# Performance work log

Measured on AMD Instinct MI355X. Metric: run time of the kernel, lower is better.

Reference implementation:

```python
import jax, jax.numpy as jnp
import numpy as np

B, S, DM, H = 8, 512, 1024, 16
D = DM // H            # head_dim = 64
NFEAT = 4              # len(feature_types)
N_DIST = 2 * 512 - 1   # max_utt_num*2-1 = 1023
N_DISC = 16 + 1        # len(DISCOURSE_RELATIONS)+1
N_COOC = 5 + 1


def setup_inputs() -> dict:
    key = jax.random.key(0)
    ks = jax.random.split(key, 24)
    inp = {}
    inp["query"] = jax.random.normal(ks[0], (B, S, DM), jnp.float32)
    inp["key"] = jax.random.normal(ks[1], (B, S, DM), jnp.float32)
    inp["value"] = jax.random.normal(ks[2], (B, S, DM), jnp.float32)
    inp["distance_adj"] = jax.random.randint(ks[3], (B, S, S), 0, N_DIST).astype(jnp.int32)
    inp["speaker_adj"] = jax.random.uniform(ks[4], (B, S, S), jnp.float32)
    inp["discourse_adj"] = jax.random.randint(ks[5], (B, S, S), 0, N_DISC).astype(jnp.int32)
    inp["cooccurrence_adj"] = jax.random.randint(ks[6], (B, S, S), 0, N_COOC).astype(jnp.int32)
    inp["mask"] = jnp.ones((B, 1, 1, S), jnp.int32)
    w = lambda k, shape: jax.random.normal(k, shape, jnp.float32) * 0.02
    inp["Wq"] = w(ks[7], (DM, DM)); inp["bq"] = jnp.zeros((DM,), jnp.float32)
    inp["Wk"] = w(ks[8], (DM, DM)); inp["bk"] = jnp.zeros((DM,), jnp.float32)
    inp["Wv"] = w(ks[9], (DM, DM)); inp["bv"] = jnp.zeros((DM,), jnp.float32)
    inp["Wo"] = w(ks[10], (DM, DM)); inp["bo"] = jnp.zeros((DM,), jnp.float32)
    inp["dist_embed"] = w(ks[11], (N_DIST, 1))
    inp["disc_embed"] = w(ks[12], (N_DISC, 1)).at[0].set(0.0)  # padding_idx=0
    inp["cooc_embed"] = w(ks[13], (N_COOC, 1)).at[0].set(0.0)  # padding_idx=0
    inp["fcw"] = w(ks[14], (H, NFEAT))       # per-head 1x1 conv weights
    inp["fcb"] = jnp.zeros((H,), jnp.float32)
    inp["cw"] = w(ks[15], (2,))              # combine conv weights
    inp["cb"] = jnp.zeros((), jnp.float32)
    return inp


def reference(query, key, value, distance_adj, speaker_adj, discourse_adj,
              cooccurrence_adj, mask, Wq, bq, Wk, bk, Wv, bv, Wo, bo,
              dist_embed, disc_embed, cooc_embed, fcw, fcb, cw, cb):
    scale = jnp.asarray(D ** 0.5, query.dtype)
    # Linear projections, split heads -> [B, H, S, D]
    split = lambda x: x.reshape(B, S, H, D).transpose(0, 2, 1, 3)
    Q = split(query @ Wq.T + bq)
    K = split(key @ Wk.T + bk)
    V = split(value @ Wv.T + bv)
    energy = jnp.einsum('bhqd,bhkd->bhqk', Q, K) / scale  # [B,H,S,S]
    # Adjacency feature maps in feature_types order: distance, speaker, discourse, cooccurrence
    dist = dist_embed[distance_adj, 0]
    disc = disc_embed[discourse_adj, 0] * (discourse_adj != 0)
    cooc = cooc_embed[cooccurrence_adj, 0] * (cooccurrence_adj != 0)
    feature_map = jnp.stack([dist, speaker_adj, disc, cooc], axis=1)  # [B,4,S,S]
    # Per-head 1x1 conv over the 4 feature channels + relu
    feat = jax.nn.relu(jnp.einsum('hc,bcij->bhij', fcw, feature_map)
                       + fcb[None, :, None, None])       # [B,H,S,S]
    # Combine conv (1x1, 2 channels -> 1) + relu
    energy = jax.nn.relu(cw[0] * energy + cw[1] * feat + cb)
    energy = jnp.where(mask == 0, -jnp.inf, energy)
    attention = jax.nn.softmax(energy, axis=-1)           # [B,H,S,S]
    x = jnp.einsum('bhqk,bhkd->bhqd', attention, V)       # dropout p=0 (eval)
    x = x.transpose(0, 2, 1, 3).reshape(B, S, DM)
    x = x @ Wo.T + bo
    return x, attention
```

## Files before the change

kernel.cpp:

```cpp
#include <hip/hip_runtime.h>

using short8 = __attribute__((ext_vector_type(8))) short;
using f32x4  = __attribute__((ext_vector_type(4))) float;
typedef unsigned short u16x4 __attribute__((ext_vector_type(4)));

__device__ __forceinline__ unsigned short f2bf(float x) {
    union { float f; unsigned u; } v; v.f = x;
    unsigned u = v.u;
    unsigned r = (u + 0x7fffu + ((u >> 16) & 1u)) >> 16;
    return (unsigned short)r;
}
__device__ __forceinline__ float bf2f(unsigned short h) {
    union { unsigned u; float f; } v; v.u = ((unsigned)h) << 16;
    return v.f;
}

__device__ __forceinline__ void async16(const void* g, void* l) {
    __builtin_amdgcn_global_load_lds(
        (const __attribute__((address_space(1))) void*)g,
        (__attribute__((address_space(3))) void*)l, 16, 0, 0);
}

__global__ __launch_bounds__(256) void cvt_qkv(
    const float* __restrict__ q, const float* __restrict__ k, const float* __restrict__ v,
    unsigned short* __restrict__ dst)
{
    int z = blockIdx.z;
    const float* src = (z == 0) ? q : ((z == 1) ? k : v);
    unsigned short* o = dst + (size_t)z * 4194304;
    size_t i = ((size_t)blockIdx.x * 256 + threadIdx.x) * 8;
    float4 a = *(const float4*)(src + i);
    float4 b = *(const float4*)(src + i + 4);
    ushort4 lo, hi;
    lo.x = f2bf(a.x); lo.y = f2bf(a.y); lo.z = f2bf(a.z); lo.w = f2bf(a.w);
    hi.x = f2bf(b.x); hi.y = f2bf(b.y); hi.z = f2bf(b.z); hi.w = f2bf(b.w);
    *(ushort4*)(o + i) = lo;
    *(ushort4*)(o + i + 4) = hi;
}

__global__ __launch_bounds__(256) void cvt_w(
    const float* __restrict__ wq, const float* __restrict__ wk,
    const float* __restrict__ wv, const float* __restrict__ wo,
    unsigned short* __restrict__ dst)
{
    int z = blockIdx.z;
    const float* src = (z == 0) ? wq : ((z == 1) ? wk : ((z == 2) ? wv : wo));
    unsigned short* o = dst + (size_t)z * 1048576;
    size_t i = ((size_t)blockIdx.x * 256 + threadIdx.x) * 8;
    float4 a = *(const float4*)(src + i);
    float4 b = *(const float4*)(src + i + 4);
    ushort4 lo, hi;
    lo.x = f2bf(a.x); lo.y = f2bf(a.y); lo.z = f2bf(a.z); lo.w = f2bf(a.w);
    hi.x = f2bf(b.x); hi.y = f2bf(b.y); hi.z = f2bf(b.z); hi.w = f2bf(b.w);
    *(ushort4*)(o + i) = lo;
    *(ushort4*)(o + i + 4) = hi;
}

__global__ __launch_bounds__(256) void feat_kernel(
    const int* __restrict__ dist_adj, const float* __restrict__ spk,
    const int* __restrict__ disc_adj, const int* __restrict__ cooc_adj,
    const float* __restrict__ dist_emb, const float* __restrict__ disc_emb,
    const float* __restrict__ cooc_emb, const float* __restrict__ fcw,
    const float* __restrict__ fcb, const float* __restrict__ cw,
    unsigned short* __restrict__ G)
{
    __shared__ float s_dist[1023];
    __shared__ float s_disc[17];
    __shared__ float s_cooc[6];
    __shared__ float s_fcw[64];
    __shared__ float s_fcb[16];
    int tid = threadIdx.x;
    for (int i = tid; i < 1023; i += 256) s_dist[i] = dist_emb[i];
    if (tid < 17) s_disc[tid] = disc_emb[tid];
    if (tid < 6)  s_cooc[tid] = cooc_emb[tid];
    if (tid < 64) s_fcw[tid]  = fcw[tid];
    if (tid < 16) s_fcb[tid]  = fcb[tid];
    __syncthreads();
    float cw1 = cw[1];

    int bx = blockIdx.x;
    int k  = (bx & 1) * 256 + tid;
    int qq = (bx >> 1) & 127;
    int b  = bx >> 8;

    size_t abase = ((size_t)b * 512 + qq * 4) * 512 + k;
    float f0[4], f1[4], f2[4], f3[4];
#pragma unroll
    for (int r = 0; r < 4; ++r) {
        size_t a = abase + (size_t)r * 512;
        int dd = dist_adj[a];
        f1[r]  = spk[a];
        int dc = disc_adj[a];
        int cc = cooc_adj[a];
        f0[r] = s_dist[dd];
        f2[r] = dc ? s_disc[dc] : 0.f;
        f3[r] = cc ? s_cooc[cc] : 0.f;
    }

    size_t gq = ((size_t)b * 16 * 128 + qq) * 512 + k;
#pragma unroll
    for (int h = 0; h < 16; ++h) {
        float w0 = s_fcw[h*4+0], w1 = s_fcw[h*4+1], w2 = s_fcw[h*4+2], w3 = s_fcw[h*4+3];
        float bb = s_fcb[h];
        ushort4 o;
        o.x = f2bf(fmaxf(w0*f0[0] + w1*f1[0] + w2*f2[0] + w3*f3[0] + bb, 0.f) * cw1);
        o.y = f2bf(fmaxf(w0*f0[1] + w1*f1[1] + w2*f2[1] + w3*f3[1] + bb, 0.f) * cw1);
        o.z = f2bf(fmaxf(w0*f0[2] + w1*f1[2] + w2*f2[2] + w3*f3[2] + bb, 0.f) * cw1);
        o.w = f2bf(fmaxf(w0*f0[3] + w1*f1[3] + w2*f2[3] + w3*f3[3] + bb, 0.f) * cw1);
        *(ushort4*)(G + (gq + (size_t)h * 65536) * 4) = o;
    }
}

template<int OMODE>
__device__ __forceinline__ void gemm_bf16_body(
    const unsigned short* __restrict__ A, const unsigned short* __restrict__ W,
    const float* __restrict__ bias, void* __restrict__ outp, int m0, int n0)
{
    __shared__ __align__(16) unsigned short As[128 * 32];
    __shared__ __align__(16) unsigned short Bs[128 * 32];
    int tid = threadIdx.x;
    int lane = tid & 63, wid = tid >> 6;
    int wx = wid & 1, wy = wid >> 1;
    int lanelo = lane & 15, hi8 = (lane >> 4) * 8;
    int rowc = lane >> 2;
    int colc = (lane & 3) * 8;

    f32x4 acc[4][4];
#pragma unroll
    for (int i = 0; i < 4; ++i)
#pragma unroll
        for (int j = 0; j < 4; ++j) {
            acc[i][j][0] = 0.f; acc[i][j][1] = 0.f; acc[i][j][2] = 0.f; acc[i][j][3] = 0.f;
        }

    for (int kk = 0; kk < 32; ++kk) {
        int k0 = kk * 32;
        __syncthreads();
#pragma unroll
        for (int p = 0; p < 2; ++p) {
            int c = 2 * wid + p;
            int row = c * 16 + rowc;
            async16(A + (size_t)(m0 + row) * 1024 + k0 + colc, As + c * 512);
        }
#pragma unroll
        for (int p = 0; p < 2; ++p) {
            int c = 2 * wid + p;
            int row = c * 16 + rowc;
            async16(W + (size_t)(n0 + row) * 1024 + k0 + colc, Bs + c * 512);
        }
        __syncthreads();

        short8 af[4], bfr[4];
#pragma unroll
        for (int i = 0; i < 4; ++i)
            af[i] = *(const short8*)(As + (wy*64 + i*16 + lanelo) * 32 + hi8);
#pragma unroll
        for (int j = 0; j < 4; ++j)
            bfr[j] = *(const short8*)(Bs + (wx*64 + j*16 + lanelo) * 32 + hi8);
#pragma unroll
        for (int i = 0; i < 4; ++i)
#pragma unroll
            for (int j = 0; j < 4; ++j)
                acc[i][j] = __builtin_amdgcn_mfma_f32_16x16x32_bf16(af[i], bfr[j], acc[i][j], 0, 0, 0);
    }

    float bia[4];
#pragma unroll
    for (int j = 0; j < 4; ++j) bia[j] = bias[n0 + wx*64 + j*16 + lanelo];
#pragma unroll
    for (int i = 0; i < 4; ++i) {
        int mbase = m0 + wy*64 + i*16 + (lane >> 4) * 4;
#pragma unroll
        for (int j = 0; j < 4; ++j) {
            int n = n0 + wx*64 + j*16 + lanelo;
#pragma unroll
            for (int r = 0; r < 4; ++r) {
                int m = mbase + r;
                float val = acc[i][j][r] + bia[j];
                if (OMODE == 0) {
                    unsigned short* o = (unsigned short*)outp;
                    o[((size_t)((m >> 9) * 16 + (n >> 6)) * 512 + (m & 511)) * 64 + (n & 63)] = f2bf(val);
                } else {
                    float* o = (float*)outp;
                    o[(size_t)m * 1024 + n] = val;
                }
            }
        }
    }
}

__global__ __launch_bounds__(256) void gemm_qkv(
    const unsigned short* __restrict__ Abf, const unsigned short* __restrict__ Wbf,
    const float* __restrict__ bq, const float* __restrict__ bk, const float* __restrict__ bv,
    unsigned short* Qb, unsigned short* Kb, unsigned short* Vb)
{
    int z = blockIdx.z;
    const unsigned short* A = Abf + (size_t)z * 4194304;
    const unsigned short* W = Wbf + (size_t)z * 1048576;
    const float* bias = (z == 0) ? bq : ((z == 1) ? bk : bv);
    unsigned short* o = (z == 0) ? Qb : ((z == 1) ? Kb : Vb);
    gemm_bf16_body<0>(A, W, bias, o, blockIdx.x * 128, blockIdx.y * 128);
}

__global__ __launch_bounds__(256) void gemm_proj(
    const unsigned short* __restrict__ xh, const unsigned short* __restrict__ Wo,
    const float* __restrict__ bo, float* __restrict__ out)
{
    gemm_bf16_body<1>(xh, Wo, bo, out, blockIdx.x * 128, blockIdx.y * 128);
}

__global__ __launch_bounds__(256) void transpose_v(const unsigned short* __restrict__ Vb,
                                                   unsigned short* __restrict__ Vt)
{
    __shared__ __align__(16) unsigned short T[64][72];
    int tid = threadIdx.x;
    int s0 = blockIdx.x * 64;
    int bh = blockIdx.z * 16 + blockIdx.y;
#pragma unroll
    for (int p = 0; p < 2; ++p) {
        int c = p * 256 + tid;
        int row = c >> 3, kc = (c & 7) * 8;
        uint4 v = *(const uint4*)(Vb + ((size_t)bh * 512 + s0 + row) * 64 + kc);
        *(uint4*)&T[row][kc] = v;
    }
    __syncthreads();
#pragma unroll
    for (int p = 0; p < 2; ++p) {
        int c = p * 256 + tid;
        int d = c >> 3, sc = (c & 7) * 8;
        unsigned vv[4];
#pragma unroll
        for (int i = 0; i < 4; ++i) {
            unsigned lo = T[sc + 2*i][d];
            unsigned hi = T[sc + 2*i + 1][d];
            vv[i] = lo | (hi << 16);
        }
        uint4 o; o.x = vv[0]; o.y = vv[1]; o.z = vv[2]; o.w = vv[3];
        *(uint4*)(Vt + ((size_t)bh * 64 + d) * 512 + s0 + sc) = o;
    }
}

__global__ __launch_bounds__(256, 2) void attn_kernel(
    const unsigned short* __restrict__ Qb, const unsigned short* __restrict__ Kb,
    const unsigned short* __restrict__ Vt, const unsigned short* __restrict__ G,
    const int* __restrict__ mask, const float* __restrict__ cw,
    const float* __restrict__ cb, float* __restrict__ attn_out,
    unsigned short* __restrict__ xh)
{
    __shared__ __align__(16) unsigned short Qs[64][72];
    __shared__ __align__(16) unsigned short Ks[128][72];
    __shared__ __align__(16) unsigned short Vs[64][40];
    __shared__ __align__(16) unsigned short Ps[4][16][40];
    __shared__ int s_mask[512];

    int tid = threadIdx.x;
    int lane = tid & 63, w = tid >> 6;
    int lanelo = lane & 15, hi8 = (lane >> 4) * 8;
    int hi2 = lane >> 4;

    int lin = blockIdx.x;
    int xcd = lin & 7;
    int s   = lin >> 3;
    int bh  = xcd * 16 + (s >> 3);
    int qt  = s & 7;
    int b   = bh >> 4, h = bh & 15;

    float qs  = cw[0] * 0.125f;
    float cbv = cb[0];

    s_mask[tid]       = mask[b * 512 + tid];
    s_mask[tid + 256] = mask[b * 512 + tid + 256];
#pragma unroll
    for (int p = 0; p < 2; ++p) {
        int c = p * 256 + tid;
        int row = c >> 3, kc = (c & 7) * 8;
        uint4 v = *(const uint4*)(Qb + ((size_t)bh * 512 + qt * 64 + row) * 64 + kc);
        *(uint4*)&Qs[row][kc] = v;
    }
    __syncthreads();

    short8 aq[2];
    aq[0] = *(const short8*)&Qs[w * 16 + lanelo][hi8];
    aq[1] = *(const short8*)&Qs[w * 16 + lanelo][32 + hi8];
    int qrow = qt * 64 + w * 16 + hi2 * 4;
    int qq   = qt * 16 + w * 4 + hi2;
    const unsigned short* gbase = G + ((size_t)bh * 128 + qq) * 2048;

    float P[32][4];
#pragma unroll
    for (int kt = 0; kt < 4; ++kt) {
        u16x4 g[8];
#pragma unroll
        for (int j = 0; j < 8; ++j)
            g[j] = __builtin_nontemporal_load(
                (const u16x4*)(gbase + (kt * 8 + j) * 64 + lanelo * 4));
        __syncthreads();
#pragma unroll
        for (int p = 0; p < 4; ++p) {
            int c = p * 256 + tid;
            int row = c >> 3, kc = (c & 7) * 8;
            uint4 v = *(const uint4*)(Kb + ((size_t)bh * 512 + kt * 128 + row) * 64 + kc);
            *(uint4*)&Ks[row][kc] = v;
        }
        __syncthreads();
#pragma unroll
        for (int j = 0; j < 8; ++j) {
            short8 b0 = *(const short8*)&Ks[j * 16 + lanelo][hi8];
            short8 b1 = *(const short8*)&Ks[j * 16 + lanelo][32 + hi8];
            f32x4 acc; acc[0] = 0.f; acc[1] = 0.f; acc[2] = 0.f; acc[3] = 0.f;
            acc = __builtin_amdgcn_mfma_f32_16x16x32_bf16(aq[0], b0, acc, 0, 0, 0);
            acc = __builtin_amdgcn_mfma_f32_16x16x32_bf16(aq[1], b1, acc, 0, 0, 0);
            int jj = kt * 8 + j;
            int kcol = jj * 16 + lanelo;
            int mk = s_mask[kcol];
            float gf[4] = { bf2f((unsigned short)g[j][0]), bf2f((unsigned short)g[j][1]),
                            bf2f((unsigned short)g[j][2]), bf2f((unsigned short)g[j][3]) };
#pragma unroll
            for (int r = 0; r < 4; ++r) {
                float e = qs * acc[r] + gf[r] + cbv;
                e = fmaxf(e, 0.f);
                P[jj][r] = mk ? __expf(e) : 0.f;
            }
        }
    }

    float inv[4];
#pragma unroll
    for (int r = 0; r < 4; ++r) {
        float s0 = 0.f;
#pragma unroll
        for (int jj = 0; jj < 32; ++jj) s0 += P[jj][r];
        s0 += __shfl_xor(s0, 1, 64);
        s0 += __shfl_xor(s0, 2, 64);
        s0 += __shfl_xor(s0, 4, 64);
        s0 += __shfl_xor(s0, 8, 64);
        inv[r] = 1.0f / s0;
    }

    {
        float* ap = attn_out + ((size_t)bh * 512 + qrow) * 512 + lanelo;
#pragma unroll
        for (int jj = 0; jj < 32; ++jj)
#pragma unroll
            for (int r = 0; r < 4; ++r)
                __builtin_nontemporal_store(P[jj][r] * inv[r],
                                            ap + (size_t)r * 512 + jj * 16);
    }

    f32x4 xacc[4];
#pragma unroll
    for (int jf = 0; jf < 4; ++jf) { xacc[jf][0]=0.f; xacc[jf][1]=0.f; xacc[jf][2]=0.f; xacc[jf][3]=0.f; }
#pragma unroll
    for (int ks = 0; ks < 16; ++ks) {
        __syncthreads();
        {
            int d = tid >> 2, kc = (tid & 3) * 8;
            uint4 v = *(const uint4*)(Vt + ((size_t)bh * 64 + d) * 512 + ks * 32 + kc);
            *(uint4*)&Vs[d][kc] = v;
        }
#pragma unroll
        for (int ff = 0; ff < 2; ++ff) {
            int f = ks * 2 + ff;
#pragma unroll
            for (int r = 0; r < 4; ++r)
                Ps[w][hi2 * 4 + r][ff * 16 + lanelo] = f2bf(P[f][r]);
        }
        __syncthreads();
        short8 ap8 = *(const short8*)&Ps[w][lanelo][hi8];
#pragma unroll
        for (int jf = 0; jf < 4; ++jf) {
            short8 bv = *(const short8*)&Vs[jf * 16 + lanelo][hi8];
            xacc[jf] = __builtin_amdgcn_mfma_f32_16x16x32_bf16(ap8, bv, xacc[jf], 0, 0, 0);
        }
    }

#pragma unroll
    for (int jf = 0; jf < 4; ++jf) {
        int d = jf * 16 + lanelo;
#pragma unroll
        for (int r = 0; r < 4; ++r) {
            float val = xacc[jf][r] * inv[r];
            xh[((size_t)b * 512 + qrow + r) * 1024 + h * 64 + d] = f2bf(val);
        }
    }
}

extern "C" void kernel_launch(void* const* d_in, const int* in_sizes, int n_in,
                              void* d_out, int out_size, void* d_ws, size_t ws_size,
                              hipStream_t stream) {
    (void)in_sizes; (void)n_in; (void)out_size; (void)ws_size;
    const float* query    = (const float*)d_in[0];
    const float* key      = (const float*)d_in[1];
    const float* value    = (const float*)d_in[2];
    const int*   dist_adj = (const int*)d_in[3];
    const float* spk      = (const float*)d_in[4];
    const int*   disc_adj = (const int*)d_in[5];
    const int*   cooc_adj = (const int*)d_in[6];
    const int*   maskp    = (const int*)d_in[7];
    const float* Wq = (const float*)d_in[8];  const float* bq = (const float*)d_in[9];
    const float* Wk = (const float*)d_in[10]; const float* bk = (const float*)d_in[11];
    const float* Wv = (const float*)d_in[12]; const float* bv = (const float*)d_in[13];
    const float* Wo = (const float*)d_in[14]; const float* bo = (const float*)d_in[15];
    const float* dist_emb = (const float*)d_in[16];
    const float* disc_emb = (const float*)d_in[17];
    const float* cooc_emb = (const float*)d_in[18];
    const float* fcw = (const float*)d_in[19];
    const float* fcb = (const float*)d_in[20];
    const float* cw  = (const float*)d_in[21];
    const float* cbp = (const float*)d_in[22];

    char* w = (char*)d_ws;
    unsigned short* Qb  = (unsigned short*)(w);
    unsigned short* Kb  = (unsigned short*)(w + 8388608);
    unsigned short* Vb  = (unsigned short*)(w + 16777216);
    unsigned short* Vt  = (unsigned short*)(w + 25165824);
    unsigned short* xh  = (unsigned short*)(w + 33554432);
    unsigned short* G   = (unsigned short*)(w + 41943040);
    unsigned short* Abf = G;
    unsigned short* Wbf = (unsigned short*)(w + 109051904);

    float* out_x    = (float*)d_out;
    float* attn_out = ((float*)d_out) + 4194304;

    cvt_qkv<<<dim3(2048, 1, 3), 256, 0, stream>>>(query, key, value, Abf);
    cvt_w<<<dim3(512, 1, 4), 256, 0, stream>>>(Wq, Wk, Wv, Wo, Wbf);
    gemm_qkv<<<dim3(32, 8, 3), 256, 0, stream>>>(Abf, Wbf, bq, bk, bv, Qb, Kb, Vb);
    transpose_v<<<dim3(8, 16, 8), 256, 0, stream>>>(Vb, Vt);
    feat_kernel<<<2048, 256, 0, stream>>>(dist_adj, spk, disc_adj, cooc_adj,
                                          dist_emb, disc_emb, cooc_emb, fcw, fcb, cw, G);
    attn_kernel<<<dim3(1024, 1, 1), 256, 0, stream>>>(Qb, Kb, Vt, G, maskp, cw, cbp,
                                                      attn_out, xh);
    gemm_proj<<<dim3(32, 8), 256, 0, stream>>>(xh, Wbf + 3145728, bo, out_x);
}
```

Baseline: 381.5 us.

## Fuse conversions, write V transposed from GEMM, async swizzled LDS loads in attention

The Q/K/V activation and weight bf16 conversions are merged into one launch. The V projection GEMM now writes V already transposed, which removes the separate transpose kernel and its extra pass over V. The attention kernel loads Q, K and V tiles with global_load_lds into XOR-swizzled, unpadded LDS and runs the P·V stage in 128-wide chunks, so it needs fewer barriers. The feature kernel uses nontemporal loads and stores. Together these cut launches and memory traffic, at the cost of more complex shared-memory aliasing between Q and V and possible async load ordering hazards.

```diff
diff --git a/kernel.cpp b/kernel.cpp
--- a/kernel.cpp
+++ b/kernel.cpp
@@ -21,32 +21,33 @@
         (__attribute__((address_space(3))) void*)l, 16, 0, 0);
 }
 
-__global__ __launch_bounds__(256) void cvt_qkv(
+__device__ __forceinline__ short8 lds_swz8(const unsigned short* base, int row,
+                                           int colbyte, int stride) {
+    const char* p = (const char*)base + row * stride + (colbyte ^ ((row & 7) << 4));
+    return *(const short8*)p;
+}
+
+__global__ __launch_bounds__(256) void cvt_all(
     const float* __restrict__ q, const float* __restrict__ k, const float* __restrict__ v,
-    unsigned short* __restrict__ dst)
-{
-    int z = blockIdx.z;
-    const float* src = (z == 0) ? q : ((z == 1) ? k : v);
-    unsigned short* o = dst + (size_t)z * 4194304;
-    size_t i = ((size_t)blockIdx.x * 256 + threadIdx.x) * 8;
-    float4 a = *(const float4*)(src + i);
-    float4 b = *(const float4*)(src + i + 4);
-    ushort4 lo, hi;
-    lo.x = f2bf(a.x); lo.y = f2bf(a.y); lo.z = f2bf(a.z); lo.w = f2bf(a.w);
-    hi.x = f2bf(b.x); hi.y = f2bf(b.y); hi.z = f2bf(b.z); hi.w = f2bf(b.w);
-    *(ushort4*)(o + i) = lo;
-    *(ushort4*)(o + i + 4) = hi;
-}
-
-__global__ __launch_bounds__(256) void cvt_w(
     const float* __restrict__ wq, const float* __restrict__ wk,
     const float* __restrict__ wv, const float* __restrict__ wo,
-    unsigned short* __restrict__ dst)
-{
-    int z = blockIdx.z;
-    const float* src = (z == 0) ? wq : ((z == 1) ? wk : ((z == 2) ? wv : wo));
-    unsigned short* o = dst + (size_t)z * 1048576;
-    size_t i = ((size_t)blockIdx.x * 256 + threadIdx.x) * 8;
+    unsigned short* __restrict__ dstA, unsigned short* __restrict__ dstW)
+{
+    int bx = blockIdx.x;
+    const float* src;
+    unsigned short* o;
+    size_t i;
+    if (bx < 6144) {
+        int z = bx >> 11;
+        src = (z == 0) ? q : ((z == 1) ? k : v);
+        o = dstA + (size_t)z * 4194304;
+        i = ((size_t)(bx & 2047) * 256 + threadIdx.x) * 8;
+    } else {
+        int z = (bx - 6144) >> 9;
+        src = (z == 0) ? wq : ((z == 1) ? wk : ((z == 2) ? wv : wo));
+        o = dstW + (size_t)z * 1048576;
+        i = ((size_t)((bx - 6144) & 511) * 256 + threadIdx.x) * 8;
+    }
     float4 a = *(const float4*)(src + i);
     float4 b = *(const float4*)(src + i + 4);
     ushort4 lo, hi;
@@ -88,10 +89,10 @@
 #pragma unroll
     for (int r = 0; r < 4; ++r) {
         size_t a = abase + (size_t)r * 512;
-        int dd = dist_adj[a];
-        f1[r]  = spk[a];
-        int dc = disc_adj[a];
-        int cc = cooc_adj[a];
+        int dd = __builtin_nontemporal_load(dist_adj + a);
+        f1[r]  = __builtin_nontemporal_load(spk + a);
+        int dc = __builtin_nontemporal_load(disc_adj + a);
+        int cc = __builtin_nontemporal_load(cooc_adj + a);
         f0[r] = s_dist[dd];
         f2[r] = dc ? s_disc[dc] : 0.f;
         f3[r] = cc ? s_cooc[cc] : 0.f;
@@ -102,12 +103,12 @@
     for (int h = 0; h < 16; ++h) {
         float w0 = s_fcw[h*4+0], w1 = s_fcw[h*4+1], w2 = s_fcw[h*4+2], w3 = s_fcw[h*4+3];
         float bb = s_fcb[h];
-        ushort4 o;
-        o.x = f2bf(fmaxf(w0*f0[0] + w1*f1[0] + w2*f2[0] + w3*f3[0] + bb, 0.f) * cw1);
-        o.y = f2bf(fmaxf(w0*f0[1] + w1*f1[1] + w2*f2[1] + w3*f3[1] + bb, 0.f) * cw1);
-        o.z = f2bf(fmaxf(w0*f0[2] + w1*f1[2] + w2*f2[2] + w3*f3[2] + bb, 0.f) * cw1);
-        o.w = f2bf(fmaxf(w0*f0[3] + w1*f1[3] + w2*f2[3] + w3*f3[3] + bb, 0.f) * cw1);
-        *(ushort4*)(G + (gq + (size_t)h * 65536) * 4) = o;
+        u16x4 o;
+        o[0] = f2bf(fmaxf(w0*f0[0] + w1*f1[0] + w2*f2[0] + w3*f3[0] + bb, 0.f) * cw1);
+        o[1] = f2bf(fmaxf(w0*f0[1] + w1*f1[1] + w2*f2[1] + w3*f3[1] + bb, 0.f) * cw1);
+        o[2] = f2bf(fmaxf(w0*f0[2] + w1*f1[2] + w2*f2[2] + w3*f3[2] + bb, 0.f) * cw1);
+        o[3] = f2bf(fmaxf(w0*f0[3] + w1*f1[3] + w2*f2[3] + w3*f3[3] + bb, 0.f) * cw1);
+        __builtin_nontemporal_store(o, (u16x4*)(G + (gq + (size_t)h * 65536) * 4));
     }
 }
 
@@ -173,16 +174,28 @@
 #pragma unroll
         for (int j = 0; j < 4; ++j) {
             int n = n0 + wx*64 + j*16 + lanelo;
-#pragma unroll
-            for (int r = 0; r < 4; ++r) {
-                int m = mbase + r;
-                float val = acc[i][j][r] + bia[j];
-                if (OMODE == 0) {
-                    unsigned short* o = (unsigned short*)outp;
-                    o[((size_t)((m >> 9) * 16 + (n >> 6)) * 512 + (m & 511)) * 64 + (n & 63)] = f2bf(val);
-                } else {
-                    float* o = (float*)outp;
-                    o[(size_t)m * 1024 + n] = val;
+            if (OMODE == 2) {
+                ushort4 o4;
+                o4.x = f2bf(acc[i][j][0] + bia[j]);
+                o4.y = f2bf(acc[i][j][1] + bia[j]);
+                o4.z = f2bf(acc[i][j][2] + bia[j]);
+                o4.w = f2bf(acc[i][j][3] + bia[j]);
+                unsigned short* o = (unsigned short*)outp;
+                size_t addr = ((size_t)((mbase >> 9) * 16 + (n >> 6)) * 64 + (n & 63)) * 512
+                              + (mbase & 511);
+                *(ushort4*)(o + addr) = o4;
+            } else {
+#pragma unroll
+                for (int r = 0; r < 4; ++r) {
+                    int m = mbase + r;
+                    float val = acc[i][j][r] + bia[j];
+                    if (OMODE == 0) {
+                        unsigned short* o = (unsigned short*)outp;
+                        o[((size_t)((m >> 9) * 16 + (n >> 6)) * 512 + (m & 511)) * 64 + (n & 63)] = f2bf(val);
+                    } else {
+                        float* o = (float*)outp;
+                        o[(size_t)m * 1024 + n] = val;
+                    }
                 }
             }
         }
@@ -192,14 +205,18 @@
 __global__ __launch_bounds__(256) void gemm_qkv(
     const unsigned short* __restrict__ Abf, const unsigned short* __restrict__ Wbf,
     const float* __restrict__ bq, const float* __restrict__ bk, const float* __restrict__ bv,
-    unsigned short* Qb, unsigned short* Kb, unsigned short* Vb)
+    unsigned short* Qb, unsigned short* Kb, unsigned short* Vt)
 {
     int z = blockIdx.z;
     const unsigned short* A = Abf + (size_t)z * 4194304;
     const unsigned short* W = Wbf + (size_t)z * 1048576;
-    const float* bias = (z == 0) ? bq : ((z == 1) ? bk : bv);
-    unsigned short* o = (z == 0) ? Qb : ((z == 1) ? Kb : Vb);
-    gemm_bf16_body<0>(A, W, bias, o, blockIdx.x * 128, blockIdx.y * 128);
+    if (z == 2) {
+        gemm_bf16_body<2>(A, W, bv, Vt, blockIdx.x * 128, blockIdx.y * 128);
+    } else {
+        const float* bias = (z == 0) ? bq : bk;
+        unsigned short* o = (z == 0) ? Qb : Kb;
+        gemm_bf16_body<0>(A, W, bias, o, blockIdx.x * 128, blockIdx.y * 128);
+    }
 }
 
 __global__ __launch_bounds__(256) void gemm_proj(
@@ -207,37 +224,6 @@
     const float* __restrict__ bo, float* __restrict__ out)
 {
     gemm_bf16_body<1>(xh, Wo, bo, out, blockIdx.x * 128, blockIdx.y * 128);
-}
-
-__global__ __launch_bounds__(256) void transpose_v(const unsigned short* __restrict__ Vb,
-                                                   unsigned short* __restrict__ Vt)
-{
-    __shared__ __align__(16) unsigned short T[64][72];
-    int tid = threadIdx.x;
-    int s0 = blockIdx.x * 64;
-    int bh = blockIdx.z * 16 + blockIdx.y;
-#pragma unroll
-    for (int p = 0; p < 2; ++p) {
-        int c = p * 256 + tid;
-        int row = c >> 3, kc = (c & 7) * 8;
-        uint4 v = *(const uint4*)(Vb + ((size_t)bh * 512 + s0 + row) * 64 + kc);
-        *(uint4*)&T[row][kc] = v;
-    }
-    __syncthreads();
-#pragma unroll
-    for (int p = 0; p < 2; ++p) {
-        int c = p * 256 + tid;
-        int d = c >> 3, sc = (c & 7) * 8;
-        unsigned vv[4];
-#pragma unroll
-        for (int i = 0; i < 4; ++i) {
-            unsigned lo = T[sc + 2*i][d];
-            unsigned hi = T[sc + 2*i + 1][d];
-            vv[i] = lo | (hi << 16);
-        }
-        uint4 o; o.x = vv[0]; o.y = vv[1]; o.z = vv[2]; o.w = vv[3];
-        *(uint4*)(Vt + ((size_t)bh * 64 + d) * 512 + s0 + sc) = o;
-    }
 }
 
 __global__ __launch_bounds__(256, 2) void attn_kernel(
@@ -247,11 +233,12 @@
     const float* __restrict__ cb, float* __restrict__ attn_out,
     unsigned short* __restrict__ xh)
 {
-    __shared__ __align__(16) unsigned short Qs[64][72];
-    __shared__ __align__(16) unsigned short Ks[128][72];
-    __shared__ __align__(16) unsigned short Vs[64][40];
-    __shared__ __align__(16) unsigned short Ps[4][16][40];
-    __shared__ int s_mask[512];
+    __shared__ __align__(16) char smem[35840];
+    unsigned short* Qs = (unsigned short*)smem;
+    unsigned short* Ks = (unsigned short*)(smem + 8192);
+    unsigned short* Vs = (unsigned short*)smem;
+    unsigned short* Ps = (unsigned short*)(smem + 16384);
+    int* s_mask = (int*)(smem + 33792);
 
     int tid = threadIdx.x;
     int lane = tid & 63, w = tid >> 6;
@@ -270,18 +257,20 @@
 
     s_mask[tid]       = mask[b * 512 + tid];
     s_mask[tid + 256] = mask[b * 512 + tid + 256];
+
+    int r8  = lane >> 3;
+    int gs8 = (lane & 7) ^ r8;
 #pragma unroll
     for (int p = 0; p < 2; ++p) {
-        int c = p * 256 + tid;
-        int row = c >> 3, kc = (c & 7) * 8;
-        uint4 v = *(const uint4*)(Qb + ((size_t)bh * 512 + qt * 64 + row) * 64 + kc);
-        *(uint4*)&Qs[row][kc] = v;
+        int row = p * 32 + w * 8 + r8;
+        async16(Qb + ((size_t)bh * 512 + qt * 64 + row) * 64 + gs8 * 8,
+                Qs + (p * 32 + w * 8) * 64);
     }
     __syncthreads();
 
     short8 aq[2];
-    aq[0] = *(const short8*)&Qs[w * 16 + lanelo][hi8];
-    aq[1] = *(const short8*)&Qs[w * 16 + lanelo][32 + hi8];
+    aq[0] = lds_swz8(Qs, w * 16 + lanelo, hi8 * 2, 128);
+    aq[1] = lds_swz8(Qs, w * 16 + lanelo, 64 + hi8 * 2, 128);
     int qrow = qt * 64 + w * 16 + hi2 * 4;
     int qq   = qt * 16 + w * 4 + hi2;
     const unsigned short* gbase = G + ((size_t)bh * 128 + qq) * 2048;
@@ -297,16 +286,15 @@
         __syncthreads();
 #pragma unroll
         for (int p = 0; p < 4; ++p) {
-            int c = p * 256 + tid;
-            int row = c >> 3, kc = (c & 7) * 8;
-            uint4 v = *(const uint4*)(Kb + ((size_t)bh * 512 + kt * 128 + row) * 64 + kc);
-            *(uint4*)&Ks[row][kc] = v;
+            int row = p * 32 + w * 8 + r8;
+            async16(Kb + ((size_t)bh * 512 + kt * 128 + row) * 64 + gs8 * 8,
+                    Ks + (p * 32 + w * 8) * 64);
         }
         __syncthreads();
 #pragma unroll
         for (int j = 0; j < 8; ++j) {
-            short8 b0 = *(const short8*)&Ks[j * 16 + lanelo][hi8];
-            short8 b1 = *(const short8*)&Ks[j * 16 + lanelo][32 + hi8];
+            short8 b0 = lds_swz8(Ks, j * 16 + lanelo, hi8 * 2, 128);
+            short8 b1 = lds_swz8(Ks, j * 16 + lanelo, 64 + hi8 * 2, 128);
             f32x4 acc; acc[0] = 0.f; acc[1] = 0.f; acc[2] = 0.f; acc[3] = 0.f;
             acc = __builtin_amdgcn_mfma_f32_16x16x32_bf16(aq[0], b0, acc, 0, 0, 0);
             acc = __builtin_amdgcn_mfma_f32_16x16x32_bf16(aq[1], b1, acc, 0, 0, 0);
@@ -350,27 +338,35 @@
     f32x4 xacc[4];
 #pragma unroll
     for (int jf = 0; jf < 4; ++jf) { xacc[jf][0]=0.f; xacc[jf][1]=0.f; xacc[jf][2]=0.f; xacc[jf][3]=0.f; }
-#pragma unroll
-    for (int ks = 0; ks < 16; ++ks) {
-        __syncthreads();
-        {
-            int d = tid >> 2, kc = (tid & 3) * 8;
-            uint4 v = *(const uint4*)(Vt + ((size_t)bh * 64 + d) * 512 + ks * 32 + kc);
-            *(uint4*)&Vs[d][kc] = v;
-        }
-#pragma unroll
-        for (int ff = 0; ff < 2; ++ff) {
-            int f = ks * 2 + ff;
+
+    int r8v  = ((w & 1) * 4 + hi2) & 7;
+    int gs16 = (lane & 15) ^ r8v;
+    unsigned short* Psw = Ps + w * 16 * 136;
+#pragma unroll
+    for (int c = 0; c < 4; ++c) {
+        __syncthreads();
+#pragma unroll
+        for (int p = 0; p < 4; ++p) {
+            int row = p * 16 + w * 4 + hi2;
+            async16(Vt + ((size_t)bh * 64 + row) * 512 + c * 128 + gs16 * 8,
+                    Vs + (p * 16 + w * 4) * 128);
+        }
+#pragma unroll
+        for (int jc = 0; jc < 8; ++jc) {
+            int jj = c * 8 + jc;
 #pragma unroll
             for (int r = 0; r < 4; ++r)
-                Ps[w][hi2 * 4 + r][ff * 16 + lanelo] = f2bf(P[f][r]);
-        }
-        __syncthreads();
-        short8 ap8 = *(const short8*)&Ps[w][lanelo][hi8];
-#pragma unroll
-        for (int jf = 0; jf < 4; ++jf) {
-            short8 bv = *(const short8*)&Vs[jf * 16 + lanelo][hi8];
-            xacc[jf] = __builtin_amdgcn_mfma_f32_16x16x32_bf16(ap8, bv, xacc[jf], 0, 0, 0);
+                Psw[(hi2 * 4 + r) * 136 + jc * 16 + lanelo] = f2bf(P[jj][r]);
+        }
+        __syncthreads();
+#pragma unroll
+        for (int ksub = 0; ksub < 4; ++ksub) {
+            short8 ap8 = *(const short8*)(Psw + (size_t)lanelo * 136 + ksub * 32 + hi8);
+#pragma unroll
+            for (int jf = 0; jf < 4; ++jf) {
+                short8 bv = lds_swz8(Vs, jf * 16 + lanelo, ksub * 64 + hi8 * 2, 256);
+                xacc[jf] = __builtin_amdgcn_mfma_f32_16x16x32_bf16(ap8, bv, xacc[jf], 0, 0, 0);
+            }
         }
     }
 
@@ -412,7 +408,6 @@
     char* w = (char*)d_ws;
     unsigned short* Qb  = (unsigned short*)(w);
     unsigned short* Kb  = (unsigned short*)(w + 8388608);
-    unsigned short* Vb  = (unsigned short*)(w + 16777216);
     unsigned short* Vt  = (unsigned short*)(w + 25165824);
     unsigned short* xh  = (unsigned short*)(w + 33554432);
     unsigned short* G   = (unsigned short*)(w + 41943040);
@@ -422,10 +417,9 @@
     float* out_x    = (float*)d_out;
     float* attn_out = ((float*)d_out) + 4194304;
 
-    cvt_qkv<<<dim3(2048, 1, 3), 256, 0, stream>>>(query, key, value, Abf);
-    cvt_w<<<dim3(512, 1, 4), 256, 0, stream>>>(Wq, Wk, Wv, Wo, Wbf);
-    gemm_qkv<<<dim3(32, 8, 3), 256, 0, stream>>>(Abf, Wbf, bq, bk, bv, Qb, Kb, Vb);
-    transpose_v<<<dim3(8, 16, 8), 256, 0, stream>>>(Vb, Vt);
+    cvt_all<<<dim3(8192, 1, 1), 256, 0, stream>>>(query, key, value, Wq, Wk, Wv, Wo,
+                                                  Abf, Wbf);
+    gemm_qkv<<<dim3(32, 8, 3), 256, 0, stream>>>(Abf, Wbf, bq, bk, bv, Qb, Kb, Vt);
     feat_kernel<<<2048, 256, 0, stream>>>(dist_adj, spk, disc_adj, cooc_adj,
                                           dist_emb, disc_emb, cooc_emb, fcw, fcb, cw, G);
     attn_kernel<<<dim3(1024, 1, 1), 256, 0, stream>>>(Qb, Kb, Vt, G, maskp, cw, cbp,
```

Measured after the change: 385.2 us. No clear change (+1.0%).
